# Kernel optimization log

Hardware: AMD Instinct MI355X
Metric: run time of the kernel (lower is better)

Reference implementation:

```python
import jax, jax.numpy as jnp
import numpy as np

M, N, K = 35637, 15872, 20
FEAT = 128
EPS = 1e-5
W0 = 1.0  # Sine frequency


def setup_inputs() -> dict:
    key = jax.random.key(0)
    ks = jax.random.split(key, 8)
    x_feat = jax.random.normal(ks[0], (1, N, FEAT), dtype=jnp.float32)
    w_up_inputs = jax.random.uniform(ks[1], (1, 7, M, K), dtype=jnp.float32)
    idx = jax.random.randint(ks[2], (1, M, K), 0, N - 1)
    conv0_w = jax.random.normal(ks[3], (128, 7), dtype=jnp.float32) * (1.0 / np.sqrt(7))
    convs_w = jax.random.normal(ks[4], (7, 128, 128), dtype=jnp.float32) * (1.0 / np.sqrt(128))
    gammas = jnp.ones((8, 128), dtype=jnp.float32)
    betas = jnp.zeros((8, 128), dtype=jnp.float32)
    final_w = jax.random.normal(ks[5], (1, 128), dtype=jnp.float32) * (1.0 / np.sqrt(128))
    final_b = jnp.zeros((1,), dtype=jnp.float32)
    return {"x_feat": x_feat, "w_up_inputs": w_up_inputs, "idx": idx,
            "conv0_w": conv0_w, "convs_w": convs_w, "gammas": gammas,
            "betas": betas, "final_w": final_w, "final_b": final_b}


def _conv_bn_sine(h, W, g, b):
    # 1x1 conv == per-point matmul over channel dim; h: (B, M, K, Cin)
    h = jnp.einsum('bmkc,oc->bmko', h, W)
    # BatchNorm2d in training mode: batch stats over (B, M, K) per channel
    mu = jnp.mean(h, axis=(0, 1, 2))
    var = jnp.var(h, axis=(0, 1, 2))
    h = (h - mu) * jax.lax.rsqrt(var + EPS) * g + b
    return jnp.sin(W0 * h)


def reference(x_feat, w_up_inputs, idx, conv0_w, convs_w, gammas, betas, final_w, final_b):
    # w_up_inputs: (B, 7, M, K) -> channels-last (B, M, K, 7)
    h = jnp.transpose(w_up_inputs, (0, 2, 3, 1))
    h = _conv_bn_sine(h, conv0_w, gammas[0], betas[0])
    for i in range(7):
        h = _conv_bn_sine(h, convs_w[i], gammas[i + 1], betas[i + 1])
    # final 1x1 conv with bias -> logits (B, M, K, 1)
    logits = jnp.einsum('bmkc,oc->bmko', h, final_w) + final_b
    w = jax.nn.softmax(logits, axis=2)  # softmax over K neighbors
    # index_points: gather x_feat[b, idx[b, m, k], :] -> (B, M, K, FEAT)
    gathered = jax.vmap(lambda pts, ix: pts[ix])(x_feat, idx)
    feat_H = jnp.sum(w * gathered, axis=2)  # (B, M, FEAT)
    return feat_H
```

## Files before the change

### kernel.cpp

```cpp
#include <hip/hip_runtime.h>

#define PP 712740
#define MM 35637
#define KK 20
#define NF 15872
#define NTILES 44547

typedef _Float16 h16;
typedef __attribute__((ext_vector_type(4))) _Float16 f16x4;
typedef __attribute__((ext_vector_type(8))) _Float16 f16x8;
typedef __attribute__((ext_vector_type(4))) float f32x4;

__global__ __launch_bounds__(256) void k_zero(double* __restrict__ gs) {
  const int t = threadIdx.x;
#pragma unroll
  for (int i = 0; i < 8; ++i) gs[i * 256 + t] = 0.0;
}

__global__ __launch_bounds__(256) void k_layer0(
    const float* __restrict__ up,
    const float* __restrict__ w0,
    h16* __restrict__ z,
    double* __restrict__ gs)
{
  __shared__ float w0s[128 * 7];
  __shared__ double red[4][256];
  const int t = threadIdx.x;
  for (int i = t; i < 128 * 7; i += 256) w0s[i] = w0[i];
  __syncthreads();

  const int w = t >> 6;
  const int lane = t & 63;
  const int ln = lane & 15;
  const int q = lane >> 4;

  float sp[32], qp[32];
#pragma unroll
  for (int i = 0; i < 32; ++i) { sp[i] = 0.f; qp[i] = 0.f; }

  const int gw = blockIdx.x * 4 + w;
  for (int tile = gw; tile < NTILES; tile += gridDim.x * 4) {
    const int p = tile * 16 + ln;
    const bool act = p < PP;
    float u[7];
#pragma unroll
    for (int c7 = 0; c7 < 7; ++c7) u[c7] = act ? up[c7 * PP + p] : 0.f;

#pragma unroll
    for (int ks = 0; ks < 4; ++ks) {
      f16x8 o;
#pragma unroll
      for (int j = 0; j < 8; ++j) {
        const int c = ks * 32 + q * 8 + j;
        float acc = 0.f;
#pragma unroll
        for (int c7 = 0; c7 < 7; ++c7) acc = fmaf(w0s[c * 7 + c7], u[c7], acc);
        o[j] = (h16)acc;
        const int si = ks * 8 + j;
        sp[si] += acc;
        qp[si] = fmaf(acc, acc, qp[si]);
      }
      if (act) *(f16x8*)(z + (size_t)p * 128 + ks * 32 + q * 8) = o;
    }
  }

#pragma unroll
  for (int i = 0; i < 32; ++i) {
#pragma unroll
    for (int d = 1; d < 16; d <<= 1) {
      sp[i] += __shfl_xor(sp[i], d, 64);
      qp[i] += __shfl_xor(qp[i], d, 64);
    }
  }
  if (ln == 0) {
#pragma unroll
    for (int ks = 0; ks < 4; ++ks)
#pragma unroll
      for (int j = 0; j < 8; ++j) {
        const int c = ks * 32 + q * 8 + j;
        red[w][c] = (double)sp[ks * 8 + j];
        red[w][128 + c] = (double)qp[ks * 8 + j];
      }
  }
  __syncthreads();
  double v = red[0][t] + red[1][t] + red[2][t] + red[3][t];
  atomicAdd(&gs[t], v);
}

__global__ __launch_bounds__(256, 4) void k_layer(
    h16* __restrict__ z,
    const double* __restrict__ gsp,
    double* __restrict__ gso,
    const float* __restrict__ W,
    const float* __restrict__ gamma,
    const float* __restrict__ beta)
{
  __shared__ h16 act[2][2048];
  __shared__ double red[256];

  const int t = threadIdx.x;
  const int w = t >> 6;
  const int lane = t & 63;
  const int ln = lane & 15;
  const int q = lane >> 4;
  const int G = (int)gridDim.x;

  float sc[8], sh[8];
  {
    const double n = (double)PP;
    const int cb = (t & 15) * 8;
#pragma unroll
    for (int j = 0; j < 8; ++j) {
      const int c = cb + j;
      const double mu = gsp[c] / n;
      const double var = gsp[128 + c] / n - mu * mu;
      const float rstd = (float)(1.0 / sqrt(var + 1e-5));
      sc[j] = rstd * gamma[c];
      sh[j] = beta[c] - (float)mu * sc[j];
    }
  }

  const int ob = w * 32;
  f16x8 wfr[2][4];
#pragma unroll
  for (int nt = 0; nt < 2; ++nt) {
    const int row_g = ob + (ln >> 2) * 8 + nt * 4 + (ln & 3);
    const float* wrow = W + (size_t)row_g * 128;
#pragma unroll
    for (int ks = 0; ks < 4; ++ks) {
      const float* src = wrow + ks * 32 + q * 8;
      const float4 aa = *(const float4*)src;
      const float4 bb = *(const float4*)(src + 4);
      f16x8 b;
      b[0] = (h16)aa.x; b[1] = (h16)aa.y; b[2] = (h16)aa.z; b[3] = (h16)aa.w;
      b[4] = (h16)bb.x; b[5] = (h16)bb.y; b[6] = (h16)bb.z; b[7] = (h16)bb.w;
      wfr[nt][ks] = b;
    }
  }

  float sp[8], qp[8];
#pragma unroll
  for (int i = 0; i < 8; ++i) { sp[i] = 0.f; qp[i] = 0.f; }

  const int pt = t >> 4;
  const size_t roff = (size_t)pt * 128 + (size_t)(t & 15) * 8;
  const int wswz = (pt * 256 + (t & 15) * 16) ^ ((pt & 7) << 4);
  int raddr[4];
#pragma unroll
  for (int ks = 0; ks < 4; ++ks)
    raddr[ks] = (ln * 256 + ks * 64 + q * 16) ^ ((ln & 7) << 4);

  int tile = blockIdx.x;
  int ib = 0;
  const int t1i = (tile + G < NTILES) ? tile + G : NTILES - 1;
  f16x8 raw = *(const f16x8*)(z + (size_t)tile * 2048 + roff);
  f16x8 rnext = *(const f16x8*)(z + (size_t)t1i * 2048 + roff);

  for (; tile < NTILES; tile += G) {
    const int t2 = (tile + 2 * G < NTILES) ? tile + 2 * G : NTILES - 1;
    const f16x8 rfar = *(const f16x8*)(z + (size_t)t2 * 2048 + roff);

    f16x8 av;
#pragma unroll
    for (int j = 0; j < 8; ++j)
      av[j] = (h16)__sinf(fmaf((float)raw[j], sc[j], sh[j]));

    *(f16x8*)((char*)(&act[ib][0]) + wswz) = av;
    asm volatile("s_waitcnt lgkmcnt(0)\n\ts_barrier" ::: "memory");

    f16x8 afr[4];
#pragma unroll
    for (int ks = 0; ks < 4; ++ks)
      afr[ks] = *(const f16x8*)((const char*)(&act[ib][0]) + raddr[ks]);

    f32x4 acc0 = (f32x4){0.f, 0.f, 0.f, 0.f};
    f32x4 acc1 = (f32x4){0.f, 0.f, 0.f, 0.f};
#pragma unroll
    for (int ks = 0; ks < 4; ++ks) {
      acc0 = __builtin_amdgcn_mfma_f32_16x16x32_f16(wfr[0][ks], afr[ks], acc0, 0, 0, 0);
      acc1 = __builtin_amdgcn_mfma_f32_16x16x32_f16(wfr[1][ks], afr[ks], acc1, 0, 0, 0);
    }

    const int p = tile * 16 + ln;
    if (p < PP) {
      f16x8 o;
      o[0] = (h16)acc0[0]; o[1] = (h16)acc0[1]; o[2] = (h16)acc0[2]; o[3] = (h16)acc0[3];
      o[4] = (h16)acc1[0]; o[5] = (h16)acc1[1]; o[6] = (h16)acc1[2]; o[7] = (h16)acc1[3];
      *(f16x8*)(z + (size_t)p * 128 + ob + q * 8) = o;
#pragma unroll
      for (int r = 0; r < 4; ++r) {
        sp[r]     += acc0[r];
        qp[r]      = fmaf(acc0[r], acc0[r], qp[r]);
        sp[4 + r] += acc1[r];
        qp[4 + r]  = fmaf(acc1[r], acc1[r], qp[4 + r]);
      }
    }
    raw = rnext;
    rnext = rfar;
    ib ^= 1;
  }

#pragma unroll
  for (int i = 0; i < 8; ++i) {
#pragma unroll
    for (int d = 1; d < 16; d <<= 1) {
      sp[i] += __shfl_xor(sp[i], d, 64);
      qp[i] += __shfl_xor(qp[i], d, 64);
    }
  }
  if (ln == 0) {
#pragma unroll
    for (int r = 0; r < 4; ++r) {
      const int c = ob + q * 8 + r;
      red[c]           = (double)sp[r];
      red[c + 4]       = (double)sp[4 + r];
      red[128 + c]     = (double)qp[r];
      red[128 + c + 4] = (double)qp[4 + r];
    }
  }
  __syncthreads();
  atomicAdd(&gso[t], red[t]);
}

__global__ __launch_bounds__(256) void k_outf(
    const h16* __restrict__ z,
    const double* __restrict__ gsp,
    const float* __restrict__ gamma,
    const float* __restrict__ beta,
    const float* __restrict__ fw,
    const float* __restrict__ fb,
    const int* __restrict__ idx,
    const float* __restrict__ xf,
    float* __restrict__ out)
{
  const int gw = (int)((blockIdx.x * 256 + threadIdx.x) >> 6);
  const int lane = (int)(threadIdx.x & 63);
  if (gw >= MM) return;
  const int m = gw;
  const int c0 = lane * 2;

  float scv[2], shv[2], fv[2];
#pragma unroll
  for (int j = 0; j < 2; ++j) {
    const int c = c0 + j;
    const double n = (double)PP;
    const double mu = gsp[c] / n;
    const double var = gsp[128 + c] / n - mu * mu;
    const float rstd = (float)(1.0 / sqrt(var + 1e-5));
    scv[j] = rstd * gamma[c];
    shv[j] = beta[c] - (float)mu * scv[j];
    fv[j] = fw[c];
  }
  const float fbv = fb[0];

  float l[KK];
#pragma unroll
  for (int k = 0; k < KK; ++k) {
    const h16* zp = z + (size_t)(m * KK + k) * 128 + c0;
    float part = fv[0] * __sinf(fmaf((float)zp[0], scv[0], shv[0]))
               + fv[1] * __sinf(fmaf((float)zp[1], scv[1], shv[1]));
#pragma unroll
    for (int d = 1; d < 64; d <<= 1) part += __shfl_xor(part, d, 64);
    l[k] = part + fbv;
  }

  float mx = l[0];
#pragma unroll
  for (int k = 1; k < KK; ++k) mx = fmaxf(mx, l[k]);
  float ssum = 0.f;
#pragma unroll
  for (int k = 0; k < KK; ++k) { l[k] = __expf(l[k] - mx); ssum += l[k]; }
  const float inv = 1.f / ssum;

  float a0 = 0.f, a1 = 0.f;
#pragma unroll
  for (int k = 0; k < KK; ++k) {
    const int r = idx[m * KK + k];
    const float wk = l[k] * inv;
    a0 = fmaf(wk, xf[r * 128 + lane], a0);
    a1 = fmaf(wk, xf[r * 128 + 64 + lane], a1);
  }
  out[m * 128 + lane] = a0;
  out[m * 128 + 64 + lane] = a1;
}

__global__ __launch_bounds__(256) void k_out(
    const float* __restrict__ logits,
    const int* __restrict__ idx,
    const float* __restrict__ xf,
    float* __restrict__ out)
{
  const int gw = (int)((blockIdx.x * 256 + threadIdx.x) >> 6);
  const int lane = threadIdx.x & 63;
  if (gw >= MM) return;
  const int m = gw;

  float l[KK];
#pragma unroll
  for (int k = 0; k < KK; ++k) l[k] = logits[m * KK + k];
  float mx = l[0];
#pragma unroll
  for (int k = 1; k < KK; ++k) mx = fmaxf(mx, l[k]);
  float ssum = 0.f;
#pragma unroll
  for (int k = 0; k < KK; ++k) { l[k] = __expf(l[k] - mx); ssum += l[k]; }
  const float inv = 1.f / ssum;

  float a0 = 0.f, a1 = 0.f;
#pragma unroll
  for (int k = 0; k < KK; ++k) {
    const int r = idx[m * KK + k];
    const float wk = l[k] * inv;
    a0 = fmaf(wk, xf[r * 128 + lane], a0);
    a1 = fmaf(wk, xf[r * 128 + 64 + lane], a1);
  }
  out[m * 128 + lane] = a0;
  out[m * 128 + 64 + lane] = a1;
}

__global__ __launch_bounds__(256) void k_chain(
    const float* __restrict__ up,
    const float* __restrict__ w0,
    const float* __restrict__ wc,
    const float* __restrict__ gam,
    const float* __restrict__ bet,
    const double* __restrict__ gs,
    double* __restrict__ gso,
    int jl, int mode,
    const float* __restrict__ fw,
    const float* __restrict__ fb,
    float* __restrict__ logits)
{
  __shared__ float sc_s[8][128], sh_s[8][128];
  __shared__ double bred[4][256];
  const int t = threadIdx.x;
  const int lane = t & 63;

  const int nbn = (mode == 0) ? jl : 8;
  for (int i = t; i < nbn * 128; i += 256) {
    const int L = i >> 7, c = i & 127;
    const double n = (double)PP;
    const double mu = gs[L * 256 + c] / n;
    const double var = gs[L * 256 + 128 + c] / n - mu * mu;
    const float rstd = (float)(1.0 / sqrt(var + 1e-5));
    const float sc = rstd * gam[L * 128 + c];
    sc_s[L][c] = sc;
    sh_s[L][c] = bet[L * 128 + c] - (float)mu * sc;
  }
  __syncthreads();

  double lS0 = 0, lS1 = 0, lQ0 = 0, lQ1 = 0;

  for (int p0 = blockIdx.x * 256; p0 < PP; p0 += gridDim.x * 256) {
    const int p = p0 + t;
    const bool act = p < PP;

    float a[128];
    {
      float u[7];
#pragma unroll
      for (int c = 0; c < 7; ++c) u[c] = act ? up[c * PP + p] : 0.f;
#pragma unroll 1
      for (int och = 0; och < 16; ++och) {
#pragma unroll
        for (int j = 0; j < 8; ++j) {
          float acc = 0.f;
#pragma unroll
          for (int c = 0; c < 7; ++c)
            acc = fmaf(w0[(och * 8 + j) * 7 + c], u[c], acc);
          a[och * 8 + j] = acc;
        }
      }
    }

#pragma unroll 1
    for (int L = 0; L < jl; ++L) {
#pragma unroll
      for (int c = 0; c < 128; ++c)
        a[c] = act ? __sinf(fmaf(a[c], sc_s[L][c], sh_s[L][c])) : 0.f;
      float b[128];
      const float* W = wc + (size_t)L * 128 * 128;
#pragma unroll 1
      for (int och = 0; och < 16; ++och) {
#pragma unroll
        for (int j = 0; j < 8; ++j) {
          float acc = 0.f;
#pragma unroll
          for (int c = 0; c < 128; ++c)
            acc = fmaf(W[(och * 8 + j) * 128 + c], a[c], acc);
          b[och * 8 + j] = acc;
        }
      }
#pragma unroll
      for (int c = 0; c < 128; ++c) a[c] = b[c];
    }

    if (mode == 0) {
#pragma unroll
      for (int o = 0; o < 128; ++o) {
        float s = a[o];
        float qv = a[o] * a[o];
#pragma unroll
        for (int d = 32; d > 0; d >>= 1) {
          s += __shfl_xor(s, d, 64);
          qv += __shfl_xor(qv, d, 64);
        }
        if ((o & 63) == lane) {
          if (o < 64) { lS0 += (double)s; lQ0 += (double)qv; }
          else        { lS1 += (double)s; lQ1 += (double)qv; }
        }
      }
    } else if (act) {
      float acc = fb[0];
#pragma unroll
      for (int c = 0; c < 128; ++c) {
        const float h = fmaf(a[c], sc_s[7][c], sh_s[7][c]);
        acc = fmaf(fw[c], __sinf(h), acc);
      }
      logits[p] = acc;
    }
  }

  if (mode == 0) {
    const int w = t >> 6;
    bred[w][lane]       = lS0;
    bred[w][64 + lane]  = lS1;
    bred[w][128 + lane] = lQ0;
    bred[w][192 + lane] = lQ1;
    __syncthreads();
    double v = bred[0][t] + bred[1][t] + bred[2][t] + bred[3][t];
    atomicAdd(&gso[t], v);
  }
}

extern "C" void kernel_launch(void* const* d_in, const int* in_sizes, int n_in,
                              void* d_out, int out_size, void* d_ws, size_t ws_size,
                              hipStream_t stream) {
  const float* xf  = (const float*)d_in[0];
  const float* up  = (const float*)d_in[1];
  const int*   idx = (const int*)d_in[2];
  const float* w0  = (const float*)d_in[3];
  const float* wc  = (const float*)d_in[4];
  const float* gam = (const float*)d_in[5];
  const float* bet = (const float*)d_in[6];
  const float* fw  = (const float*)d_in[7];
  const float* fb  = (const float*)d_in[8];
  float* out = (float*)d_out;

  char* ws = (char*)d_ws;
  const size_t zb     = (size_t)PP * 128 * sizeof(h16);
  const size_t statsb = 8 * 256 * sizeof(double);
  const size_t logb   = (size_t)PP * sizeof(float);
  const int NB = 1024;
  const int nbo = (MM + 3) / 4;

  if (ws_size >= zb + statsb + logb) {
    h16* z = (h16*)ws;
    double* gs = (double*)(ws + zb);

    k_zero<<<1, 256, 0, stream>>>(gs);
    k_layer0<<<NB, 256, 0, stream>>>(up, w0, z, gs);
    for (int i = 1; i <= 7; ++i) {
      k_layer<<<NB, 256, 0, stream>>>(z,
                                      gs + (size_t)(i - 1) * 256,
                                      gs + (size_t)i * 256,
                                      wc + (size_t)(i - 1) * 128 * 128,
                                      gam + (size_t)(i - 1) * 128,
                                      bet + (size_t)(i - 1) * 128);
    }
    k_outf<<<nbo, 256, 0, stream>>>(z, gs + 7 * 256, gam + 7 * 128,
                                    bet + 7 * 128, fw, fb, idx, xf, out);
  } else {
    double* gs = (double*)ws;
    float* logits = (float*)(ws + statsb);

    k_zero<<<1, 256, 0, stream>>>(gs);
    for (int j = 0; j <= 7; ++j) {
      k_chain<<<NB, 256, 0, stream>>>(up, w0, wc, gam, bet, gs,
                                      gs + (size_t)j * 256, j, 0,
                                      fw, fb, logits);
    }
    k_chain<<<NB, 256, 0, stream>>>(up, w0, wc, gam, bet, gs,
                                    nullptr, 7, 1, fw, fb, logits);
    k_out<<<nbo, 256, 0, stream>>>(logits, idx, xf, out);
  }
}
```

Before: 802.5 us.

## Process four 16-point tiles per barrier in the layer kernel

The 128x128 layer kernel now handles super-tiles of 64 points: it applies BN+sine to four 16-row tiles into a larger LDS buffer, syncs once, then runs four MFMA sub-tiles. The next super-tile's data is loaded from global memory right after the current one is written to LDS. This replaces the two-deep per-tile prefetch with a one-deep, four-wide prefetch. The goal is to cut barrier count per point and put more loads in flight. The cost is four times the LDS and higher register use, so occupancy is lowered to 3 blocks per CU. Tail reads past the end rely on the p<PP guard, and the last super-tile may read out of range.

```diff
diff --git a/kernel.cpp b/kernel.cpp
--- a/kernel.cpp
+++ b/kernel.cpp
@@ -5,6 +5,7 @@
 #define KK 20
 #define NF 15872
 #define NTILES 44547
+#define NSUPER 11137
 
 typedef _Float16 h16;
 typedef __attribute__((ext_vector_type(4))) _Float16 f16x4;
@@ -87,7 +88,7 @@
   atomicAdd(&gs[t], v);
 }
 
-__global__ __launch_bounds__(256, 4) void k_layer(
+__global__ __launch_bounds__(256, 3) void k_layer(
     h16* __restrict__ z,
     const double* __restrict__ gsp,
     double* __restrict__ gso,
@@ -95,7 +96,7 @@
     const float* __restrict__ gamma,
     const float* __restrict__ beta)
 {
-  __shared__ h16 act[2][2048];
+  __shared__ h16 act[2][8192];
   __shared__ double red[256];
 
   const int t = threadIdx.x;
@@ -142,61 +143,73 @@
 #pragma unroll
   for (int i = 0; i < 8; ++i) { sp[i] = 0.f; qp[i] = 0.f; }
 
-  const int pt = t >> 4;
-  const size_t roff = (size_t)pt * 128 + (size_t)(t & 15) * 8;
-  const int wswz = (pt * 256 + (t & 15) * 16) ^ ((pt & 7) << 4);
+  const size_t roff = (size_t)(t >> 4) * 128 + (size_t)(t & 15) * 8;
+  const int wbase = ((t >> 4) * 256 + (t & 15) * 16) ^ (((t >> 4) & 7) << 4);
   int raddr[4];
 #pragma unroll
   for (int ks = 0; ks < 4; ++ks)
     raddr[ks] = (ln * 256 + ks * 64 + q * 16) ^ ((ln & 7) << 4);
 
-  int tile = blockIdx.x;
+  int stile = blockIdx.x;
+  f16x8 raw[4];
+  {
+    const h16* src = z + (size_t)stile * 8192 + roff;
+#pragma unroll
+    for (int s = 0; s < 4; ++s) raw[s] = *(const f16x8*)(src + s * 2048);
+  }
   int ib = 0;
-  const int t1i = (tile + G < NTILES) ? tile + G : NTILES - 1;
-  f16x8 raw = *(const f16x8*)(z + (size_t)tile * 2048 + roff);
-  f16x8 rnext = *(const f16x8*)(z + (size_t)t1i * 2048 + roff);
-
-  for (; tile < NTILES; tile += G) {
-    const int t2 = (tile + 2 * G < NTILES) ? tile + 2 * G : NTILES - 1;
-    const f16x8 rfar = *(const f16x8*)(z + (size_t)t2 * 2048 + roff);
-
-    f16x8 av;
-#pragma unroll
-    for (int j = 0; j < 8; ++j)
-      av[j] = (h16)__sinf(fmaf((float)raw[j], sc[j], sh[j]));
-
-    *(f16x8*)((char*)(&act[ib][0]) + wswz) = av;
+
+  for (; stile < NSUPER; stile += G) {
+    char* ab = (char*)(&act[ib][0]);
+
+#pragma unroll
+    for (int s = 0; s < 4; ++s) {
+      f16x8 av;
+#pragma unroll
+      for (int j = 0; j < 8; ++j)
+        av[j] = (h16)__sinf(fmaf((float)raw[s][j], sc[j], sh[j]));
+      *(f16x8*)(ab + (wbase + s * 4096)) = av;
+    }
+
+    {
+      const int nxt = (stile + G < NSUPER) ? stile + G : NSUPER - 1;
+      const h16* src = z + (size_t)nxt * 8192 + roff;
+#pragma unroll
+      for (int s = 0; s < 4; ++s) raw[s] = *(const f16x8*)(src + s * 2048);
+    }
+
     asm volatile("s_waitcnt lgkmcnt(0)\n\ts_barrier" ::: "memory");
 
-    f16x8 afr[4];
-#pragma unroll
-    for (int ks = 0; ks < 4; ++ks)
-      afr[ks] = *(const f16x8*)((const char*)(&act[ib][0]) + raddr[ks]);
-
-    f32x4 acc0 = (f32x4){0.f, 0.f, 0.f, 0.f};
-    f32x4 acc1 = (f32x4){0.f, 0.f, 0.f, 0.f};
-#pragma unroll
-    for (int ks = 0; ks < 4; ++ks) {
-      acc0 = __builtin_amdgcn_mfma_f32_16x16x32_f16(wfr[0][ks], afr[ks], acc0, 0, 0, 0);
-      acc1 = __builtin_amdgcn_mfma_f32_16x16x32_f16(wfr[1][ks], afr[ks], acc1, 0, 0, 0);
-    }
-
-    const int p = tile * 16 + ln;
-    if (p < PP) {
-      f16x8 o;
-      o[0] = (h16)acc0[0]; o[1] = (h16)acc0[1]; o[2] = (h16)acc0[2]; o[3] = (h16)acc0[3];
-      o[4] = (h16)acc1[0]; o[5] = (h16)acc1[1]; o[6] = (h16)acc1[2]; o[7] = (h16)acc1[3];
-      *(f16x8*)(z + (size_t)p * 128 + ob + q * 8) = o;
-#pragma unroll
-      for (int r = 0; r < 4; ++r) {
-        sp[r]     += acc0[r];
-        qp[r]      = fmaf(acc0[r], acc0[r], qp[r]);
-        sp[4 + r] += acc1[r];
-        qp[4 + r]  = fmaf(acc1[r], acc1[r], qp[4 + r]);
-      }
-    }
-    raw = rnext;
-    rnext = rfar;
+#pragma unroll
+    for (int ot = 0; ot < 4; ++ot) {
+      f16x8 afr[4];
+#pragma unroll
+      for (int ks = 0; ks < 4; ++ks)
+        afr[ks] = *(const f16x8*)(ab + (ot * 4096 + raddr[ks]));
+
+      f32x4 acc0 = (f32x4){0.f, 0.f, 0.f, 0.f};
+      f32x4 acc1 = (f32x4){0.f, 0.f, 0.f, 0.f};
+#pragma unroll
+      for (int ks = 0; ks < 4; ++ks) {
+        acc0 = __builtin_amdgcn_mfma_f32_16x16x32_f16(wfr[0][ks], afr[ks], acc0, 0, 0, 0);
+        acc1 = __builtin_amdgcn_mfma_f32_16x16x32_f16(wfr[1][ks], afr[ks], acc1, 0, 0, 0);
+      }
+
+      const int p = stile * 64 + ot * 16 + ln;
+      if (p < PP) {
+        f16x8 o;
+        o[0] = (h16)acc0[0]; o[1] = (h16)acc0[1]; o[2] = (h16)acc0[2]; o[3] = (h16)acc0[3];
+        o[4] = (h16)acc1[0]; o[5] = (h16)acc1[1]; o[6] = (h16)acc1[2]; o[7] = (h16)acc1[3];
+        *(f16x8*)(z + (size_t)p * 128 + ob + q * 8) = o;
+#pragma unroll
+        for (int r = 0; r < 4; ++r) {
+          sp[r]     += acc0[r];
+          qp[r]      = fmaf(acc0[r], acc0[r], qp[r]);
+          sp[4 + r] += acc1[r];
+          qp[4 + r]  = fmaf(acc1[r], acc1[r], qp[4 + r]);
+        }
+      }
+    }
     ib ^= 1;
   }
 
```

Measured after the change: 827.7 us. 3.1% more time.
